# Kernel optimization log

Hardware: AMD Instinct MI355X
Metric: run time of the kernel (lower is better)

## Reference

```python
import jax, jax.numpy as jnp
import numpy as np

D_MODEL = 256
NUM_HEADS = 8
CURV = 1.0  # Poincare ball curvature c
EPS = 1e-5


def expmap0(v, c):
    # Exponential map at the origin of the Poincare ball.
    sqrt_c = jnp.sqrt(c)
    norm = jnp.sqrt(jnp.clip(jnp.sum(v * v, axis=-1, keepdims=True), 1e-12))
    return jnp.tanh(sqrt_c * norm) * v / (sqrt_c * norm)


def setup_inputs() -> dict:
    key = jax.random.key(0)
    ks = jax.random.split(key, 12)
    B, S, D = 2, 2048, D_MODEL
    s = 1.0 / np.sqrt(D)
    return {
        "x": jax.random.normal(ks[0], (B, S, D), dtype=jnp.float32),
        "Wq": jax.random.normal(ks[1], (D, D), dtype=jnp.float32) * s,
        "bq": jnp.zeros((D,), jnp.float32),
        "Wk": jax.random.normal(ks[2], (D, D), dtype=jnp.float32) * s,
        "bk": jnp.zeros((D,), jnp.float32),
        "Wv": jax.random.normal(ks[3], (D, D), dtype=jnp.float32) * s,
        "bv": jnp.zeros((D,), jnp.float32),
        "Wo": jax.random.normal(ks[4], (D, D), dtype=jnp.float32) * s,
        "bo": jnp.zeros((D,), jnp.float32),
        "Wfc": jax.random.normal(ks[5], (D, D), dtype=jnp.float32) * s,
        "bfc": jnp.zeros((D,), jnp.float32),
    }


def reference(x, Wq, bq, Wk, bk, Wv, bv, Wo, bo, Wfc, bfc):
    B, S, D = x.shape
    H, dh = NUM_HEADS, D // NUM_HEADS
    c = CURV

    def proj(W, b):
        return (x @ W.T + b).reshape(B, S, H, dh).transpose(0, 2, 1, 3)  # [B,H,S,dh]

    q = expmap0(proj(Wq, bq), c)
    k = expmap0(proj(Wk, bk), c)
    v = proj(Wv, bv)

    # Gram quantities; pairwise Poincare distance via closed-form Mobius-add norm.
    qq = jnp.sum(q * q, axis=-1)[..., :, None]          # [B,H,S,1]
    kk = jnp.sum(k * k, axis=-1)[..., None, :]          # [B,H,1,S]
    qk = jnp.einsum("bhsd,bhtd->bhst", q, k)            # [B,H,S,S]

    A = 1.0 - 2.0 * c * qk + c * kk
    Bc = 1.0 - c * qq
    den = 1.0 - 2.0 * c * qk + (c * c) * qq * kk
    num2 = A * A * qq + Bc * Bc * kk - 2.0 * A * Bc * qk  # ||(-q) mobius+ k||^2 * den^2
    n = jnp.sqrt(jnp.clip(num2, 0.0)) / jnp.clip(jnp.abs(den), 1e-12)
    sqrt_c = jnp.sqrt(c)
    dist = (2.0 / sqrt_c) * jnp.arctanh(jnp.clip(sqrt_c * n, 0.0, 1.0 - EPS))

    scores = -dist / np.sqrt(dh)
    attn = jax.nn.softmax(scores, axis=-1)
    out = jnp.einsum("bhst,bhtd->bhsd", attn, v)        # [B,H,S,dh]
    out = out.transpose(0, 2, 1, 3).reshape(B, S, D)
    out = out @ Wo.T + bo
    return out @ Wfc.T + bfc
```

## Files before the change

### kernel.cpp

```cpp
#include <hip/hip_runtime.h>
#include <cstdint>
#include <cstddef>


#define ALPHA 0.17677669529663687f
#define EMIN  -3.1129694f
#define CHI   1.95e-5f

typedef __bf16 bf16x8 __attribute__((ext_vector_type(8)));
typedef float  f32x4  __attribute__((ext_vector_type(4)));

__device__ __forceinline__ float fast_log2(float x) { return __builtin_amdgcn_logf(x); }
__device__ __forceinline__ float fast_exp2(float x) { return __builtin_amdgcn_exp2f(x); }

__device__ __forceinline__ void load_lds16(const void* g, void* l) {
  __builtin_amdgcn_global_load_lds((const __attribute__((address_space(1))) void*)g,
                                   (__attribute__((address_space(3))) void*)l, 16, 0, 0);
}

__device__ __forceinline__ void gemm_tile_nt(const float* __restrict__ A,
                                             const float* __restrict__ W,
                                             int m0, int n0,
                                             float (*AsT)[68], float (*WsT)[68],
                                             float acc[4][4]) {
  const int tid = threadIdx.x;
  const int ty = tid >> 4, tx = tid & 15;
  for (int k0 = 0; k0 < 256; k0 += 32) {
#pragma unroll
    for (int jj = 0; jj < 2; ++jj) {
      int j = tid * 2 + jj;
      int r = j >> 3;
      int c4 = (j & 7) << 2;
      float4 av = *(const float4*)&A[(size_t)(m0 + r) * 256 + k0 + c4];
      float4 wv = *(const float4*)&W[(size_t)(n0 + r) * 256 + k0 + c4];
      AsT[c4 + 0][r] = av.x; AsT[c4 + 1][r] = av.y;
      AsT[c4 + 2][r] = av.z; AsT[c4 + 3][r] = av.w;
      WsT[c4 + 0][r] = wv.x; WsT[c4 + 1][r] = wv.y;
      WsT[c4 + 2][r] = wv.z; WsT[c4 + 3][r] = wv.w;
    }
    __syncthreads();
#pragma unroll
    for (int kk = 0; kk < 32; ++kk) {
      float4 a = *(const float4*)&AsT[kk][ty * 4];
      float4 b = *(const float4*)&WsT[kk][tx * 4];
      float av[4] = {a.x, a.y, a.z, a.w};
      float bv[4] = {b.x, b.y, b.z, b.w};
#pragma unroll
      for (int i = 0; i < 4; ++i)
#pragma unroll
        for (int j = 0; j < 4; ++j)
          acc[i][j] = fmaf(av[i], bv[j], acc[i][j]);
    }
    __syncthreads();
  }
}

__global__ __launch_bounds__(256)
void gemm_qkv(const float* __restrict__ x,
              const float* __restrict__ Wq, const float* __restrict__ bq,
              const float* __restrict__ Wk, const float* __restrict__ bk,
              const float* __restrict__ Wv, const float* __restrict__ bv,
              float* __restrict__ Qb, float* __restrict__ Kb, float* __restrict__ Vb) {
  __shared__ float AsT[32][68];
  __shared__ float WsT[32][68];
  const int wsel = blockIdx.y >> 2;
  const float* W    = wsel == 0 ? Wq : (wsel == 1 ? Wk : Wv);
  const float* bias = wsel == 0 ? bq : (wsel == 1 ? bk : bv);
  float* C          = wsel == 0 ? Qb : (wsel == 1 ? Kb : Vb);
  const int m0 = blockIdx.x * 64;
  const int n0 = (blockIdx.y & 3) * 64;
  float acc[4][4] = {};
  gemm_tile_nt(x, W, m0, n0, AsT, WsT, acc);
  const int ty = threadIdx.x >> 4, tx = threadIdx.x & 15;
#pragma unroll
  for (int i = 0; i < 4; ++i) {
    int m = m0 + ty * 4 + i;
    float4 o;
    o.x = acc[i][0] + bias[n0 + tx * 4 + 0];
    o.y = acc[i][1] + bias[n0 + tx * 4 + 1];
    o.z = acc[i][2] + bias[n0 + tx * 4 + 2];
    o.w = acc[i][3] + bias[n0 + tx * 4 + 3];
    int n = n0 + tx * 4;
    int h = n >> 5, d = n & 31;
    int b = m >> 11, s = m & 2047;
    *(float4*)&C[((size_t)((b << 3) + h) << 16) + (size_t)s * 32 + d] = o;
  }
}

__global__ __launch_bounds__(256)
void gemm64(const float* __restrict__ A, const float* __restrict__ W,
            const float* __restrict__ bias, float* __restrict__ C, int ldc) {
  __shared__ float AsT[32][68];
  __shared__ float WsT[32][68];
  const int m0 = blockIdx.x * 64;
  const int n0 = blockIdx.y * 64;
  float acc[4][4] = {};
  gemm_tile_nt(A, W, m0, n0, AsT, WsT, acc);
  const int ty = threadIdx.x >> 4, tx = threadIdx.x & 15;
#pragma unroll
  for (int i = 0; i < 4; ++i) {
    int m = m0 + ty * 4 + i;
    float4 o;
    o.x = acc[i][0] + bias[n0 + tx * 4 + 0];
    o.y = acc[i][1] + bias[n0 + tx * 4 + 1];
    o.z = acc[i][2] + bias[n0 + tx * 4 + 2];
    o.w = acc[i][3] + bias[n0 + tx * 4 + 3];
    *(float4*)&C[(size_t)m * ldc + n0 + tx * 4] = o;
  }
}

__global__ __launch_bounds__(256)
void gemm_nn_small(const float* __restrict__ Afc, const float* __restrict__ Bo,
                   float* __restrict__ C) {
  __shared__ float AsT[32][68];
  __shared__ float Bs[32][68];
  const int tid = threadIdx.x;
  const int ty = tid >> 4, tx = tid & 15;
  const int m0 = blockIdx.x * 64;
  const int n0 = blockIdx.y * 64;
  float acc[4][4] = {};
  for (int k0 = 0; k0 < 256; k0 += 32) {
#pragma unroll
    for (int jj = 0; jj < 2; ++jj) {
      int j = tid * 2 + jj;
      {
        int r = j >> 3, c4 = (j & 7) << 2;
        float4 av = *(const float4*)&Afc[(size_t)(m0 + r) * 256 + k0 + c4];
        AsT[c4 + 0][r] = av.x; AsT[c4 + 1][r] = av.y;
        AsT[c4 + 2][r] = av.z; AsT[c4 + 3][r] = av.w;
      }
      {
        int r = j >> 4, c4 = (j & 15) << 2;
        *(float4*)&Bs[r][c4] = *(const float4*)&Bo[(size_t)(k0 + r) * 256 + n0 + c4];
      }
    }
    __syncthreads();
#pragma unroll
    for (int kk = 0; kk < 32; ++kk) {
      float4 a = *(const float4*)&AsT[kk][ty * 4];
      float4 b = *(const float4*)&Bs[kk][tx * 4];
      float av[4] = {a.x, a.y, a.z, a.w};
      float bv[4] = {b.x, b.y, b.z, b.w};
#pragma unroll
      for (int i = 0; i < 4; ++i)
#pragma unroll
        for (int j2 = 0; j2 < 4; ++j2)
          acc[i][j2] = fmaf(av[i], bv[j2], acc[i][j2]);
    }
    __syncthreads();
  }
#pragma unroll
  for (int i = 0; i < 4; ++i) {
    float4 o = {acc[i][0], acc[i][1], acc[i][2], acc[i][3]};
    *(float4*)&C[(size_t)(m0 + ty * 4 + i) * 256 + n0 + tx * 4] = o;
  }
}

__global__ __launch_bounds__(256)
void bcomb_k(const float* __restrict__ Wfc, const float* __restrict__ bo,
             const float* __restrict__ bfc, float* __restrict__ bcomb) {
  __shared__ float red[256];
  int r = threadIdx.x >> 4, c = threadIdx.x & 15;
  int row = blockIdx.x * 16 + r;
  float s = 0.0f;
  for (int k = c; k < 256; k += 16) s = fmaf(Wfc[(size_t)row * 256 + k], bo[k], s);
  red[threadIdx.x] = s;
  __syncthreads();
  if (c == 0) {
    float t = 0.0f;
#pragma unroll
    for (int i = 0; i < 16; ++i) t += red[r * 16 + i];
    bcomb[row] = t + bfc[row];
  }
}

__global__ __launch_bounds__(256)
void prep_qk(const float* __restrict__ Qf, const float* __restrict__ Kf,
             __bf16* __restrict__ Qbf, __bf16* __restrict__ Kbf,
             float4* __restrict__ qtab4, float4* __restrict__ ktab4) {
  int idx = blockIdx.x * 256 + threadIdx.x;
  const bool isQ = idx < 32768;
  const int i2 = isQ ? idx : idx - 32768;
  const float* src = (isQ ? Qf : Kf) + (size_t)i2 * 32;
  __bf16* dst = (isQ ? Qbf : Kbf) + (size_t)i2 * 32;
  float v[32];
  float ss = 0.0f;
#pragma unroll
  for (int i = 0; i < 8; ++i) {
    float4 v4 = *(const float4*)&src[i * 4];
    v[i*4+0] = v4.x; v[i*4+1] = v4.y; v[i*4+2] = v4.z; v[i*4+3] = v4.w;
    ss = fmaf(v4.x, v4.x, ss); ss = fmaf(v4.y, v4.y, ss);
    ss = fmaf(v4.z, v4.z, ss); ss = fmaf(v4.w, v4.w, ss);
  }
  ss = fmaxf(ss, 1e-12f);
  float x  = sqrtf(ss);
  float ex = fast_exp2(-2.8853900817779268f * x);
  float opex = 1.0f + ex;
  float th = (1.0f - ex) / opex;
  float sc = th / x;
  float qq = th * th;
  float Bv = 4.0f * ex / (opex * opex);
  float lgB = 2.0f - 2.8853900817779268f * x - 2.0f * fast_log2(opex);
  if (isQ) qtab4[i2] = float4{qq, ALPHA * lgB, Bv, 0.0f};
  else     ktab4[i2] = float4{qq, Bv, ALPHA * lgB, 0.0f};
  union { __bf16 h[8]; uint4 u; } pk;
#pragma unroll
  for (int blk = 0; blk < 4; ++blk) {
#pragma unroll
    for (int j = 0; j < 8; ++j) pk.h[j] = (__bf16)(v[blk * 8 + j] * sc);
    *(uint4*)(dst + blk * 8) = pk.u;
  }
}

__global__ __launch_bounds__(256)
void prep_vt(const float* __restrict__ Vf, __bf16* __restrict__ Vt) {
  int g = blockIdx.x * 256 + threadIdx.x;
  int bh = g >> 13, rem = g & 8191;
  int tb = rem >> 5, dh = rem & 31;
  const float* src = Vf + (((size_t)bh * 2048 + tb * 8) * 32) + dh;
  union { __bf16 h[8]; uint4 u; } pk;
#pragma unroll
  for (int e = 0; e < 8; ++e) pk.h[e] = (__bf16)src[e * 32];
  *(uint4*)(Vt + ((size_t)bh * 32 + dh) * 2048 + tb * 8) = pk.u;
}

__global__ __launch_bounds__(256)
void vsum_k(const __bf16* __restrict__ Vt, float* __restrict__ Vsum) {
  int g = blockIdx.x * 256 + threadIdx.x;
  int bh = g >> 11, rem = g & 2047;
  int t32 = rem >> 5, dh = rem & 31;
  const __bf16* src = Vt + ((size_t)bh * 32 + dh) * 2048 + t32 * 32;
  float s = 0.0f;
#pragma unroll
  for (int i = 0; i < 4; ++i) {
    bf16x8 v = *(const bf16x8*)&src[i * 8];
#pragma unroll
    for (int j = 0; j < 8; ++j) s += (float)v[j];
  }
  Vsum[((size_t)bh * 64 + t32) * 32 + dh] = s;
}

__global__ __launch_bounds__(256)
void attn_mfma(const __bf16* __restrict__ Qbf, const __bf16* __restrict__ Kbf,
               const __bf16* __restrict__ Vt,  const float4* __restrict__ qtab4,
               const float4* __restrict__ ktab4, const float* __restrict__ Vsum,
               float* __restrict__ PN, float* __restrict__ PD) {
  __shared__ __bf16 Kst[2048];
  __shared__ float4 Tst[64];
  __shared__ __bf16 Pt[4][16][72];
  const int tid = threadIdx.x;
  const int wid = tid >> 6, lane = tid & 63;
  const int l15 = lane & 15, lg = lane >> 4;
  const int tc = blockIdx.y, bh = blockIdx.z;
  const int sblk = blockIdx.x;
  const int s0 = sblk * 64 + wid * 16;

  bf16x8 qfrag = *(const bf16x8*)(Qbf + ((size_t)bh * 2048 + s0 + l15) * 32 + lg * 8);
  float4 qt = qtab4[bh * 2048 + s0 + l15];
  const float qq = qt.x, Bq = qt.z;
  const float eminRow = EMIN - qt.y;
  const float wclipf = (float)(__bf16)fast_exp2(eminRow);
  float wrow[4];
#pragma unroll
  for (int r = 0; r < 4; ++r)
    wrow[r] = (float)(__bf16)fast_exp2(EMIN - qtab4[bh * 2048 + s0 + lg * 4 + r].y);

  const __bf16* Kbase = Kbf + ((size_t)bh << 16);
  const __bf16* Vbase = Vt + ((size_t)bh << 16);
  const float4* Tbase = ktab4 + bh * 2048;
  const float*  VsBase = Vsum + (size_t)bh * 64 * 32;
  __bf16* Pw = &Pt[wid][0][0];

  f32x4 accO0 = {0.f, 0.f, 0.f, 0.f};
  f32x4 accO1 = {0.f, 0.f, 0.f, 0.f};
  float den = 0.0f;
  const f32x4 zero = {0.f, 0.f, 0.f, 0.f};
  const int tbeg = tc * 512;
  const int stag = sblk & 7;

  for (int i = 0; i < 8; ++i) {
    const int t0 = tbeg + (((i + stag) & 7) << 6);
    __syncthreads();
    {
      int slot = wid * 64 + lane;
      int gch = slot ^ ((slot >> 2) & 3);
      load_lds16(Kbase + (size_t)t0 * 32 + gch * 8, &Kst[wid * 512]);
      if (wid == 0) load_lds16(Tbase + t0 + lane, &Tst[0]);
    }
    __syncthreads();

#pragma unroll
    for (int h = 0; h < 2; ++h) {
      f32x4 S[2];
      bool ok = true;
#pragma unroll
      for (int s2 = 0; s2 < 2; ++s2) {
        const int sub = h * 2 + s2;
        const int R = sub * 16 + l15;
        const int slotR = R * 4 + (lg ^ (R & 3));
        bf16x8 kfrag = *(const bf16x8*)&Kst[slotR * 8];
        f32x4 Sv = __builtin_amdgcn_mfma_f32_16x16x32_bf16(kfrag, qfrag, zero, 0, 0, 0);
        S[s2] = Sv;
        const int tk = sub * 16 + lg * 4;
#pragma unroll
        for (int r = 0; r < 4; ++r) {
          float2 T2 = *(const float2*)&Tst[tk + r];
          float d = fmaf(qq, T2.x, 1.0f) - (Sv[r] + Sv[r]);
          ok &= (fmaf(-CHI, d, Bq * T2.y) <= 0.0f);
        }
      }
      if (__all((int)ok)) {
        const int ti32 = (t0 >> 5) + h;
        float vsA = VsBase[ti32 * 32 + l15];
        float vsB = VsBase[ti32 * 32 + 16 + l15];
        den += 8.0f * wclipf;
#pragma unroll
        for (int r = 0; r < 4; ++r) {
          accO0[r] = fmaf(wrow[r], vsA, accO0[r]);
          accO1[r] = fmaf(wrow[r], vsB, accO1[r]);
        }
      } else {
#pragma unroll
        for (int s2 = 0; s2 < 2; ++s2) {
          const int sub = h * 2 + s2;
          const int tk = sub * 16 + lg * 4;
          f32x4 Sv = S[s2];
          float w[4];
#pragma unroll
          for (int r = 0; r < 4; ++r) {
            float4 T = Tst[tk + r];
            float qk2 = Sv[r] + Sv[r];
            float u = (qq + T.x) - qk2;
            float d = fmaf(qq, T.x, 1.0f) - qk2;
            float p = fmaxf(u * d, 0.0f);
            float sq = sqrtf(p);
            float m = fmaf(2.0f, sq, u + d);
            float e = fmaf(-ALPHA, fast_log2(m), T.z);
            e = fmaxf(e, eminRow);
            w[r] = fast_exp2(e);
          }
          den += (w[0] + w[1]) + (w[2] + w[3]);
          union { __bf16 hh[4]; uint2 u2; } pk;
          pk.hh[0] = (__bf16)w[0]; pk.hh[1] = (__bf16)w[1];
          pk.hh[2] = (__bf16)w[2]; pk.hh[3] = (__bf16)w[3];
          *(uint2*)&Pw[l15 * 72 + sub * 16 + lg * 4] = pk.u2;
        }
        bf16x8 pfrag = *(const bf16x8*)&Pw[l15 * 72 + h * 32 + lg * 8];
        bf16x8 v0 = *(const bf16x8*)(Vbase + (size_t)l15 * 2048 + t0 + h * 32 + lg * 8);
        bf16x8 v1 = *(const bf16x8*)(Vbase + (size_t)(16 + l15) * 2048 + t0 + h * 32 + lg * 8);
        accO0 = __builtin_amdgcn_mfma_f32_16x16x32_bf16(pfrag, v0, accO0, 0, 0, 0);
        accO1 = __builtin_amdgcn_mfma_f32_16x16x32_bf16(pfrag, v1, accO1, 0, 0, 0);
      }
    }
  }
  den += __shfl_xor(den, 16);
  den += __shfl_xor(den, 32);
  size_t pbase = ((size_t)tc * 16 + bh) * 2048;
  if (lg == 0) PD[pbase + s0 + l15] = den;
#pragma unroll
  for (int r = 0; r < 4; ++r) {
    int sl = lg * 4 + r;
    size_t row = (pbase + s0 + sl) * 32;
    PN[row + l15]      = accO0[r];
    PN[row + 16 + l15] = accO1[r];
  }
}

__global__ __launch_bounds__(256)
void combine4(const float* __restrict__ PN, const float* __restrict__ PD,
              float* __restrict__ AO) {
  int idx = blockIdx.x * 256 + threadIdx.x;
  int bh = idx >> 11, s = idx & 2047;
  int b = bh >> 3, h = bh & 7;
  float den = 0.0f;
#pragma unroll
  for (int c = 0; c < 4; ++c) den += PD[((size_t)c * 16 + bh) * 2048 + s];
  float r = 1.0f / den;
  size_t ob = ((size_t)b * 2048 + s) * 256 + h * 32;
#pragma unroll
  for (int i = 0; i < 8; ++i) {
    float4 sum = {0.0f, 0.0f, 0.0f, 0.0f};
#pragma unroll
    for (int c = 0; c < 4; ++c) {
      float4 v = *(const float4*)&PN[((((size_t)c * 16 + bh) * 2048 + s) * 32) + i * 4];
      sum.x += v.x; sum.y += v.y; sum.z += v.z; sum.w += v.w;
    }
    sum.x *= r; sum.y *= r; sum.z *= r; sum.w *= r;
    *(float4*)&AO[ob + i * 4] = sum;
  }
}

extern "C" void kernel_launch(void* const* d_in, const int* in_sizes, int n_in,
                              void* d_out, int out_size, void* d_ws, size_t ws_size,
                              hipStream_t stream) {
  const float* x   = (const float*)d_in[0];
  const float* Wq  = (const float*)d_in[1];
  const float* bq  = (const float*)d_in[2];
  const float* Wk  = (const float*)d_in[3];
  const float* bk  = (const float*)d_in[4];
  const float* Wv  = (const float*)d_in[5];
  const float* bv  = (const float*)d_in[6];
  const float* Wo  = (const float*)d_in[7];
  const float* bo  = (const float*)d_in[8];
  const float* Wfc = (const float*)d_in[9];
  const float* bfc = (const float*)d_in[10];

  float* ws = (float*)d_ws;
  float* Qb  = ws;
  float* Kb  = ws + (1 << 20);
  float* Vb  = ws + (2 << 20);
  __bf16* Qbf = (__bf16*)(ws + (3 << 20));
  __bf16* Kbf = (__bf16*)(ws + (3 << 20) + (1 << 19));
  __bf16* Vtb = (__bf16*)(ws + (4 << 20));
  float4* qtab4 = (float4*)(ws + (4 << 20) + (1 << 19));
  float4* ktab4 = (float4*)(ws + (4 << 20) + (1 << 19) + (1 << 17));
  float*  Vsum  = ws + (4 << 20) + (1 << 19) + (2 << 17);
  float* Wcomb  = Vsum + (1 << 15);
  float* bcomb  = Wcomb + (1 << 16);
  float* PN = ws + (5 << 20);
  float* PD = ws + (9 << 20);
  float* AO = Qb;

  dim3 blk(256);
  gemm_qkv<<<dim3(64, 12), blk, 0, stream>>>(x, Wq, bq, Wk, bk, Wv, bv, Qb, Kb, Vb);
  prep_qk<<<dim3(256), blk, 0, stream>>>(Qb, Kb, Qbf, Kbf, qtab4, ktab4);
  prep_vt<<<dim3(512), blk, 0, stream>>>(Vb, Vtb);
  vsum_k<<<dim3(128), blk, 0, stream>>>(Vtb, Vsum);
  gemm_nn_small<<<dim3(4, 4), blk, 0, stream>>>(Wfc, Wo, Wcomb);
  bcomb_k<<<dim3(16), blk, 0, stream>>>(Wfc, bo, bfc, bcomb);
  attn_mfma<<<dim3(32, 4, 16), blk, 0, stream>>>(Qbf, Kbf, Vtb, qtab4, ktab4, Vsum, PN, PD);
  combine4<<<dim3(128), blk, 0, stream>>>(PN, PD, AO);
  gemm64<<<dim3(64, 4), blk, 0, stream>>>(AO, Wcomb, bcomb, (float*)d_out, 256);
}
```

Before: 117.5 us.

## Use split-bf16 MFMA for projection GEMMs and double-buffer K tiles in attention

Replaces the fp32 LDS-tiled SIMT GEMMs for the QKV and output projections with MFMA GEMMs that emulate fp32 accuracy by splitting each operand into bf16 high and low parts (three MFMAs per product). A new split kernel converts x and the weights, and combine4 and the Wcomb kernel now emit split bf16 outputs. Separately, attention double-buffers its K and table tiles in LDS so the next tile's load overlaps current compute, removing one barrier per iteration. This costs an extra launch and conversion traffic, plus uncoalesced scalar stores in the MFMA GEMM epilogues.

```diff
diff --git a/kernel.cpp b/kernel.cpp
--- a/kernel.cpp
+++ b/kernel.cpp
@@ -18,100 +18,132 @@
                                    (__attribute__((address_space(3))) void*)l, 16, 0, 0);
 }
 
-__device__ __forceinline__ void gemm_tile_nt(const float* __restrict__ A,
-                                             const float* __restrict__ W,
-                                             int m0, int n0,
-                                             float (*AsT)[68], float (*WsT)[68],
-                                             float acc[4][4]) {
-  const int tid = threadIdx.x;
-  const int ty = tid >> 4, tx = tid & 15;
+__global__ __launch_bounds__(256)
+void split_all(const float* __restrict__ x, const float* __restrict__ Wq,
+               const float* __restrict__ Wk, const float* __restrict__ Wv,
+               __bf16* __restrict__ xh, __bf16* __restrict__ xl,
+               __bf16* __restrict__ Ws) {
+  int g = blockIdx.x * 256 + threadIdx.x;
+  const float* src;
+  __bf16 *dh, *dl;
+  if (g < 131072) {
+    src = x + (size_t)g * 8; dh = xh + (size_t)g * 8; dl = xl + (size_t)g * 8;
+  } else {
+    int e = g - 131072;
+    int wsel = e >> 13;
+    int inner = (e & 8191) * 8;
+    src = (wsel == 0 ? Wq : (wsel == 1 ? Wk : Wv)) + inner;
+    dh = Ws + wsel * 131072 + inner;
+    dl = Ws + wsel * 131072 + 65536 + inner;
+  }
+  union { __bf16 h[8]; uint4 u; } ph, pl;
+#pragma unroll
+  for (int i = 0; i < 2; ++i) {
+    float4 v = *(const float4*)(src + i * 4);
+    float vv[4] = {v.x, v.y, v.z, v.w};
+#pragma unroll
+    for (int j = 0; j < 4; ++j) {
+      __bf16 hb = (__bf16)vv[j];
+      ph.h[i * 4 + j] = hb;
+      pl.h[i * 4 + j] = (__bf16)(vv[j] - (float)hb);
+    }
+  }
+  *(uint4*)dh = ph.u;
+  *(uint4*)dl = pl.u;
+}
+
+__global__ __launch_bounds__(256)
+void gemm_qkv_mfma(const __bf16* __restrict__ xh, const __bf16* __restrict__ xl,
+                   const __bf16* __restrict__ Ws,
+                   const float* __restrict__ bq, const float* __restrict__ bk,
+                   const float* __restrict__ bv,
+                   float* __restrict__ Qb, float* __restrict__ Kb,
+                   float* __restrict__ Vb) {
+  const int tid = threadIdx.x, w = tid >> 6, lane = tid & 63;
+  const int l15 = lane & 15, lg = lane >> 4;
+  const int m0 = blockIdx.x * 64, nb = blockIdx.y;
+  const int wsel = nb >> 2;
+  const int n256b = (nb & 3) * 64;
+  const __bf16* Wh = Ws + wsel * 131072;
+  const __bf16* Wl = Wh + 65536;
+  const int arow = m0 + w * 16 + l15;
+  const __bf16* axh = xh + (size_t)arow * 256 + lg * 8;
+  const __bf16* axl = xl + (size_t)arow * 256 + lg * 8;
+  f32x4 acc0 = {0,0,0,0}, acc1 = {0,0,0,0}, acc2 = {0,0,0,0}, acc3 = {0,0,0,0};
+#pragma unroll
   for (int k0 = 0; k0 < 256; k0 += 32) {
-#pragma unroll
-    for (int jj = 0; jj < 2; ++jj) {
-      int j = tid * 2 + jj;
-      int r = j >> 3;
-      int c4 = (j & 7) << 2;
-      float4 av = *(const float4*)&A[(size_t)(m0 + r) * 256 + k0 + c4];
-      float4 wv = *(const float4*)&W[(size_t)(n0 + r) * 256 + k0 + c4];
-      AsT[c4 + 0][r] = av.x; AsT[c4 + 1][r] = av.y;
-      AsT[c4 + 2][r] = av.z; AsT[c4 + 3][r] = av.w;
-      WsT[c4 + 0][r] = wv.x; WsT[c4 + 1][r] = wv.y;
-      WsT[c4 + 2][r] = wv.z; WsT[c4 + 3][r] = wv.w;
-    }
-    __syncthreads();
-#pragma unroll
-    for (int kk = 0; kk < 32; ++kk) {
-      float4 a = *(const float4*)&AsT[kk][ty * 4];
-      float4 b = *(const float4*)&WsT[kk][tx * 4];
-      float av[4] = {a.x, a.y, a.z, a.w};
-      float bv[4] = {b.x, b.y, b.z, b.w};
-#pragma unroll
-      for (int i = 0; i < 4; ++i)
-#pragma unroll
-        for (int j = 0; j < 4; ++j)
-          acc[i][j] = fmaf(av[i], bv[j], acc[i][j]);
-    }
-    __syncthreads();
-  }
-}
-
-__global__ __launch_bounds__(256)
-void gemm_qkv(const float* __restrict__ x,
-              const float* __restrict__ Wq, const float* __restrict__ bq,
-              const float* __restrict__ Wk, const float* __restrict__ bk,
-              const float* __restrict__ Wv, const float* __restrict__ bv,
-              float* __restrict__ Qb, float* __restrict__ Kb, float* __restrict__ Vb) {
-  __shared__ float AsT[32][68];
-  __shared__ float WsT[32][68];
-  const int wsel = blockIdx.y >> 2;
-  const float* W    = wsel == 0 ? Wq : (wsel == 1 ? Wk : Wv);
+    bf16x8 ah = *(const bf16x8*)(axh + k0);
+    bf16x8 al = *(const bf16x8*)(axl + k0);
+#pragma unroll
+    for (int g = 0; g < 4; ++g) {
+      const size_t br = (size_t)(n256b + g * 16 + l15) * 256 + lg * 8 + k0;
+      bf16x8 bh = *(const bf16x8*)(Wh + br);
+      bf16x8 bl = *(const bf16x8*)(Wl + br);
+      f32x4& acc = g == 0 ? acc0 : (g == 1 ? acc1 : (g == 2 ? acc2 : acc3));
+      acc = __builtin_amdgcn_mfma_f32_16x16x32_bf16(ah, bh, acc, 0, 0, 0);
+      acc = __builtin_amdgcn_mfma_f32_16x16x32_bf16(al, bh, acc, 0, 0, 0);
+      acc = __builtin_amdgcn_mfma_f32_16x16x32_bf16(ah, bl, acc, 0, 0, 0);
+    }
+  }
   const float* bias = wsel == 0 ? bq : (wsel == 1 ? bk : bv);
-  float* C          = wsel == 0 ? Qb : (wsel == 1 ? Kb : Vb);
-  const int m0 = blockIdx.x * 64;
-  const int n0 = (blockIdx.y & 3) * 64;
-  float acc[4][4] = {};
-  gemm_tile_nt(x, W, m0, n0, AsT, WsT, acc);
-  const int ty = threadIdx.x >> 4, tx = threadIdx.x & 15;
-#pragma unroll
-  for (int i = 0; i < 4; ++i) {
-    int m = m0 + ty * 4 + i;
-    float4 o;
-    o.x = acc[i][0] + bias[n0 + tx * 4 + 0];
-    o.y = acc[i][1] + bias[n0 + tx * 4 + 1];
-    o.z = acc[i][2] + bias[n0 + tx * 4 + 2];
-    o.w = acc[i][3] + bias[n0 + tx * 4 + 3];
-    int n = n0 + tx * 4;
-    int h = n >> 5, d = n & 31;
-    int b = m >> 11, s = m & 2047;
-    *(float4*)&C[((size_t)((b << 3) + h) << 16) + (size_t)s * 32 + d] = o;
-  }
-}
-
-__global__ __launch_bounds__(256)
-void gemm64(const float* __restrict__ A, const float* __restrict__ W,
-            const float* __restrict__ bias, float* __restrict__ C, int ldc) {
-  __shared__ float AsT[32][68];
-  __shared__ float WsT[32][68];
-  const int m0 = blockIdx.x * 64;
-  const int n0 = blockIdx.y * 64;
-  float acc[4][4] = {};
-  gemm_tile_nt(A, W, m0, n0, AsT, WsT, acc);
-  const int ty = threadIdx.x >> 4, tx = threadIdx.x & 15;
-#pragma unroll
-  for (int i = 0; i < 4; ++i) {
-    int m = m0 + ty * 4 + i;
-    float4 o;
-    o.x = acc[i][0] + bias[n0 + tx * 4 + 0];
-    o.y = acc[i][1] + bias[n0 + tx * 4 + 1];
-    o.z = acc[i][2] + bias[n0 + tx * 4 + 2];
-    o.w = acc[i][3] + bias[n0 + tx * 4 + 3];
-    *(float4*)&C[(size_t)m * ldc + n0 + tx * 4] = o;
+  float* C = wsel == 0 ? Qb : (wsel == 1 ? Kb : Vb);
+#pragma unroll
+  for (int g = 0; g < 4; ++g) {
+    const f32x4& acc = g == 0 ? acc0 : (g == 1 ? acc1 : (g == 2 ? acc2 : acc3));
+    int n256 = n256b + g * 16 + l15;
+    float bval = bias[n256];
+    int h = n256 >> 5, d = n256 & 31;
+#pragma unroll
+    for (int r = 0; r < 4; ++r) {
+      int m = m0 + w * 16 + lg * 4 + r;
+      int b = m >> 11, s = m & 2047;
+      C[((size_t)((b << 3) + h) << 16) + (size_t)s * 32 + d] = acc[r] + bval;
+    }
+  }
+}
+
+__global__ __launch_bounds__(256)
+void gemm_out_mfma(const __bf16* __restrict__ aoh, const __bf16* __restrict__ aol,
+                   const __bf16* __restrict__ Wch, const __bf16* __restrict__ Wcl,
+                   const float* __restrict__ bcomb, float* __restrict__ out) {
+  const int tid = threadIdx.x, w = tid >> 6, lane = tid & 63;
+  const int l15 = lane & 15, lg = lane >> 4;
+  const int m0 = blockIdx.x * 64, n0 = blockIdx.y * 64;
+  const int arow = m0 + w * 16 + l15;
+  const __bf16* axh = aoh + (size_t)arow * 256 + lg * 8;
+  const __bf16* axl = aol + (size_t)arow * 256 + lg * 8;
+  f32x4 acc0 = {0,0,0,0}, acc1 = {0,0,0,0}, acc2 = {0,0,0,0}, acc3 = {0,0,0,0};
+#pragma unroll
+  for (int k0 = 0; k0 < 256; k0 += 32) {
+    bf16x8 ah = *(const bf16x8*)(axh + k0);
+    bf16x8 al = *(const bf16x8*)(axl + k0);
+#pragma unroll
+    for (int g = 0; g < 4; ++g) {
+      const size_t br = (size_t)(n0 + g * 16 + l15) * 256 + lg * 8 + k0;
+      bf16x8 bh = *(const bf16x8*)(Wch + br);
+      bf16x8 bl = *(const bf16x8*)(Wcl + br);
+      f32x4& acc = g == 0 ? acc0 : (g == 1 ? acc1 : (g == 2 ? acc2 : acc3));
+      acc = __builtin_amdgcn_mfma_f32_16x16x32_bf16(ah, bh, acc, 0, 0, 0);
+      acc = __builtin_amdgcn_mfma_f32_16x16x32_bf16(al, bh, acc, 0, 0, 0);
+      acc = __builtin_amdgcn_mfma_f32_16x16x32_bf16(ah, bl, acc, 0, 0, 0);
+    }
+  }
+#pragma unroll
+  for (int g = 0; g < 4; ++g) {
+    const f32x4& acc = g == 0 ? acc0 : (g == 1 ? acc1 : (g == 2 ? acc2 : acc3));
+    int n = n0 + g * 16 + l15;
+    float bval = bcomb[n];
+#pragma unroll
+    for (int r = 0; r < 4; ++r) {
+      int m = m0 + w * 16 + lg * 4 + r;
+      out[(size_t)m * 256 + n] = acc[r] + bval;
+    }
   }
 }
 
 __global__ __launch_bounds__(256)
 void gemm_nn_small(const float* __restrict__ Afc, const float* __restrict__ Bo,
-                   float* __restrict__ C) {
+                   __bf16* __restrict__ Ch, __bf16* __restrict__ Cl) {
   __shared__ float AsT[32][68];
   __shared__ float Bs[32][68];
   const int tid = threadIdx.x;
@@ -151,8 +183,16 @@
   }
 #pragma unroll
   for (int i = 0; i < 4; ++i) {
-    float4 o = {acc[i][0], acc[i][1], acc[i][2], acc[i][3]};
-    *(float4*)&C[(size_t)(m0 + ty * 4 + i) * 256 + n0 + tx * 4] = o;
+    union { __bf16 h[4]; uint2 u; } ph, pl;
+#pragma unroll
+    for (int j = 0; j < 4; ++j) {
+      __bf16 hb = (__bf16)acc[i][j];
+      ph.h[j] = hb;
+      pl.h[j] = (__bf16)(acc[i][j] - (float)hb);
+    }
+    size_t off = (size_t)(m0 + ty * 4 + i) * 256 + n0 + tx * 4;
+    *(uint2*)(Ch + off) = ph.u;
+    *(uint2*)(Cl + off) = pl.u;
   }
 }
 
@@ -245,8 +285,8 @@
                const __bf16* __restrict__ Vt,  const float4* __restrict__ qtab4,
                const float4* __restrict__ ktab4, const float* __restrict__ Vsum,
                float* __restrict__ PN, float* __restrict__ PD) {
-  __shared__ __bf16 Kst[2048];
-  __shared__ float4 Tst[64];
+  __shared__ __bf16 Kst[2][2048];
+  __shared__ float4 Tst[2][64];
   __shared__ __bf16 Pt[4][16][72];
   const int tid = threadIdx.x;
   const int wid = tid >> 6, lane = tid & 63;
@@ -278,16 +318,26 @@
   const int tbeg = tc * 512;
   const int stag = sblk & 7;
 
+  const int slot = wid * 64 + lane;
+  const int gch = slot ^ ((slot >> 2) & 3);
+
+  {
+    const int t0 = tbeg + ((stag & 7) << 6);
+    load_lds16(Kbase + (size_t)t0 * 32 + gch * 8, &Kst[0][wid * 512]);
+    if (wid == 0) load_lds16(Tbase + t0 + lane, &Tst[0][0]);
+  }
+  int cur = 0;
+
   for (int i = 0; i < 8; ++i) {
+    __syncthreads();
+    if (i < 7) {
+      const int tn = tbeg + (((i + 1 + stag) & 7) << 6);
+      load_lds16(Kbase + (size_t)tn * 32 + gch * 8, &Kst[cur ^ 1][wid * 512]);
+      if (wid == 0) load_lds16(Tbase + tn + lane, &Tst[cur ^ 1][0]);
+    }
     const int t0 = tbeg + (((i + stag) & 7) << 6);
-    __syncthreads();
-    {
-      int slot = wid * 64 + lane;
-      int gch = slot ^ ((slot >> 2) & 3);
-      load_lds16(Kbase + (size_t)t0 * 32 + gch * 8, &Kst[wid * 512]);
-      if (wid == 0) load_lds16(Tbase + t0 + lane, &Tst[0]);
-    }
-    __syncthreads();
+    const __bf16* Kc = &Kst[cur][0];
+    const float4* Tc = &Tst[cur][0];
 
 #pragma unroll
     for (int h = 0; h < 2; ++h) {
@@ -298,13 +348,13 @@
         const int sub = h * 2 + s2;
         const int R = sub * 16 + l15;
         const int slotR = R * 4 + (lg ^ (R & 3));
-        bf16x8 kfrag = *(const bf16x8*)&Kst[slotR * 8];
+        bf16x8 kfrag = *(const bf16x8*)&Kc[slotR * 8];
         f32x4 Sv = __builtin_amdgcn_mfma_f32_16x16x32_bf16(kfrag, qfrag, zero, 0, 0, 0);
         S[s2] = Sv;
         const int tk = sub * 16 + lg * 4;
 #pragma unroll
         for (int r = 0; r < 4; ++r) {
-          float2 T2 = *(const float2*)&Tst[tk + r];
+          float2 T2 = *(const float2*)&Tc[tk + r];
           float d = fmaf(qq, T2.x, 1.0f) - (Sv[r] + Sv[r]);
           ok &= (fmaf(-CHI, d, Bq * T2.y) <= 0.0f);
         }
@@ -328,7 +378,7 @@
           float w[4];
 #pragma unroll
           for (int r = 0; r < 4; ++r) {
-            float4 T = Tst[tk + r];
+            float4 T = Tc[tk + r];
             float qk2 = Sv[r] + Sv[r];
             float u = (qq + T.x) - qk2;
             float d = fmaf(qq, T.x, 1.0f) - qk2;
@@ -352,6 +402,7 @@
         accO1 = __builtin_amdgcn_mfma_f32_16x16x32_bf16(pfrag, v1, accO1, 0, 0, 0);
       }
     }
+    cur ^= 1;
   }
   den += __shfl_xor(den, 16);
   den += __shfl_xor(den, 32);
@@ -368,7 +419,7 @@
 
 __global__ __launch_bounds__(256)
 void combine4(const float* __restrict__ PN, const float* __restrict__ PD,
-              float* __restrict__ AO) {
+              __bf16* __restrict__ AOh, __bf16* __restrict__ AOl) {
   int idx = blockIdx.x * 256 + threadIdx.x;
   int bh = idx >> 11, s = idx & 2047;
   int b = bh >> 3, h = bh & 7;
@@ -385,8 +436,16 @@
       float4 v = *(const float4*)&PN[((((size_t)c * 16 + bh) * 2048 + s) * 32) + i * 4];
       sum.x += v.x; sum.y += v.y; sum.z += v.z; sum.w += v.w;
     }
-    sum.x *= r; sum.y *= r; sum.z *= r; sum.w *= r;
-    *(float4*)&AO[ob + i * 4] = sum;
+    float vv[4] = {sum.x * r, sum.y * r, sum.z * r, sum.w * r};
+    union { __bf16 h4[4]; uint2 u; } ph, pl;
+#pragma unroll
+    for (int j = 0; j < 4; ++j) {
+      __bf16 hb = (__bf16)vv[j];
+      ph.h4[j] = hb;
+      pl.h4[j] = (__bf16)(vv[j] - (float)hb);
+    }
+    *(uint2*)(AOh + ob + i * 4) = ph.u;
+    *(uint2*)(AOl + ob + i * 4) = pl.u;
   }
 }
 
@@ -415,20 +474,26 @@
   float4* qtab4 = (float4*)(ws + (4 << 20) + (1 << 19));
   float4* ktab4 = (float4*)(ws + (4 << 20) + (1 << 19) + (1 << 17));
   float*  Vsum  = ws + (4 << 20) + (1 << 19) + (2 << 17);
-  float* Wcomb  = Vsum + (1 << 15);
-  float* bcomb  = Wcomb + (1 << 16);
-  float* PN = ws + (5 << 20);
-  float* PD = ws + (9 << 20);
-  float* AO = Qb;
+  __bf16* Wch   = (__bf16*)(ws + (4 << 20) + (1 << 19) + (2 << 17) + (1 << 15));
+  __bf16* Wcl   = Wch + 65536;
+  float*  bcomb = ws + (4 << 20) + (1 << 19) + (2 << 17) + (1 << 15) + (1 << 16);
+  __bf16* xh = (__bf16*)(ws + (5 << 20));
+  __bf16* xl = (__bf16*)(ws + (5 << 20) + (1 << 19));
+  __bf16* Wsplit = (__bf16*)(ws + (6 << 20));
+  float* PN = ws + (6 << 20) + (1 << 18);
+  float* PD = PN + (4 << 20);
+  __bf16* AOh = (__bf16*)ws;
+  __bf16* AOl = (__bf16*)(ws + (1 << 19));
 
   dim3 blk(256);
-  gemm_qkv<<<dim3(64, 12), blk, 0, stream>>>(x, Wq, bq, Wk, bk, Wv, bv, Qb, Kb, Vb);
+  split_all<<<dim3(608), blk, 0, stream>>>(x, Wq, Wk, Wv, xh, xl, Wsplit);
+  gemm_qkv_mfma<<<dim3(64, 12), blk, 0, stream>>>(xh, xl, Wsplit, bq, bk, bv, Qb, Kb, Vb);
   prep_qk<<<dim3(256), blk, 0, stream>>>(Qb, Kb, Qbf, Kbf, qtab4, ktab4);
   prep_vt<<<dim3(512), blk, 0, stream>>>(Vb, Vtb);
   vsum_k<<<dim3(128), blk, 0, stream>>>(Vtb, Vsum);
-  gemm_nn_small<<<dim3(4, 4), blk, 0, stream>>>(Wfc, Wo, Wcomb);
+  gemm_nn_small<<<dim3(4, 4), blk, 0, stream>>>(Wfc, Wo, Wch, Wcl);
   bcomb_k<<<dim3(16), blk, 0, stream>>>(Wfc, bo, bfc, bcomb);
   attn_mfma<<<dim3(32, 4, 16), blk, 0, stream>>>(Qbf, Kbf, Vtb, qtab4, ktab4, Vsum, PN, PD);
-  combine4<<<dim3(128), blk, 0, stream>>>(PN, PD, AO);
-  gemm64<<<dim3(64, 4), blk, 0, stream>>>(AO, Wcomb, bcomb, (float*)d_out, 256);
-}
+  combine4<<<dim3(128), blk, 0, stream>>>(PN, PD, AOh, AOl);
+  gemm_out_mfma<<<dim3(64, 4), blk, 0, stream>>>(AOh, AOl, Wch, Wcl, bcomb, (float*)d_out);
+}
```

Result: slower. 123.3 us (+5.0%).
